# Performance work log

Measured on AMD Instinct MI355X. Metric: run time of the kernel, lower is better.

Reference implementation:

```python
import jax, jax.numpy as jnp
import numpy as np

B, S, E, H, BS = 4, 4096, 1024, 1024, 128  # batch, seq, embed, head_size, block_size


def setup_inputs() -> dict:
    key = jax.random.key(0)
    k1, k2, k3, k4 = jax.random.split(key, 4)
    x = jax.random.normal(k1, (B, S, E), dtype=jnp.float32)
    W_qkv = jax.random.normal(k2, (E, 3 * H), dtype=jnp.float32) * (E ** -0.5)
    W_out = jax.random.normal(k3, (H, H), dtype=jnp.float32) * (H ** -0.5)
    b_out = jax.random.normal(k4, (H,), dtype=jnp.float32) * 0.01
    return {"x": x, "W_qkv": W_qkv, "W_out": W_out, "b_out": b_out}


def reference(x, W_qkv, W_out, b_out):
    b, s, e = x.shape
    h = W_out.shape[1]
    nb = s // BS  # number of blocks (block-diagonal attention)
    qkv = x @ W_qkv                      # [B, S, 3H]
    q, k, v = jnp.split(qkv, 3, axis=-1)

    def blk(t):
        return t.reshape(b, nb, BS, h)   # [B, nb, BS, H]

    scale = h ** -0.5
    # each query block attends only its own key/value block
    scores = jnp.einsum('bnqd,bnkd->bnqk', blk(q), blk(k)) * scale  # [B, nb, BS, BS]
    causal = jnp.tril(jnp.ones((BS, BS), dtype=bool))  # diagonal block of full tril
    scores = jnp.where(causal, scores, -jnp.inf)
    scores = scores - jnp.max(scores, axis=-1, keepdims=True)
    p = jnp.exp(scores)
    p = p / (jnp.sum(p, axis=-1, keepdims=True) + 1e-6)  # faithful: softmax with +1e-6 eps
    out = jnp.einsum('bnqk,bnkd->bnqd', p, blk(v)).reshape(b, s, h)
    return out @ W_out.T + b_out
```

## Files before the change

### kernel.cpp

```cpp
#include <hip/hip_runtime.h>
#include <hip/hip_bf16.h>

typedef __attribute__((ext_vector_type(8))) short short8;
typedef __attribute__((ext_vector_type(4))) float float4_;

typedef const __attribute__((address_space(1))) void* gas_t;
typedef __attribute__((address_space(3))) void* las_t;

__device__ __forceinline__ void gl_lds16(const void* g, void* l) {
  __builtin_amdgcn_global_load_lds((gas_t)g, (las_t)l, 16, 0, 0);
}

__device__ __forceinline__ short f2b(float f) {
  union { __hip_bfloat16 h; short s; } u;
  u.h = __float2bfloat16(f);
  return u.s;
}
__device__ __forceinline__ short8 cvt8(float4_ lo, float4_ hi) {
  short8 r;
#pragma unroll
  for (int t = 0; t < 4; t++) { r[t] = f2b(lo[t]); r[t + 4] = f2b(hi[t]); }
  return r;
}

__global__ __launch_bounds__(256) void prep(
    const float* __restrict__ Wqkv, short* __restrict__ WqkvT,
    const float* __restrict__ Wout, short* __restrict__ Woutb,
    const float* __restrict__ x, short* __restrict__ xb, int has_x)
{
  __shared__ __align__(16) short T[64 * 72];
  const int b   = blockIdx.x;
  const int tid = threadIdx.x;
  if (b < 768) {
    const int R = 1024, C = 3072;
    const int r0 = (b / 48) * 64;
    const int c0 = (b % 48) * 64;
    const int r  = tid >> 2;
    const int cp = (tid & 3) * 16;
#pragma unroll
    for (int g = 0; g < 4; g++) {
      float4_ v = *(const float4_*)&Wqkv[(long)(r0 + r) * C + c0 + cp + g * 4];
#pragma unroll
      for (int t = 0; t < 4; t++) T[(cp + g * 4 + t) * 72 + r] = f2b(v[t]);
    }
    __syncthreads();
    const int c  = tid >> 2;
    const int rp = (tid & 3) * 16;
    short8 w0 = *(const short8*)&T[c * 72 + rp];
    short8 w1 = *(const short8*)&T[c * 72 + rp + 8];
    *(short8*)&WqkvT[(long)(c0 + c) * R + r0 + rp] = w0;
    *(short8*)&WqkvT[(long)(c0 + c) * R + r0 + rp + 8] = w1;
  } else if (b < 1280) {
    const long i = ((long)(b - 768) * 256 + tid) * 8;
    float4_ lo = *(const float4_*)&Wout[i];
    float4_ hi = *(const float4_*)&Wout[i + 4];
    *(short8*)&Woutb[i] = cvt8(lo, hi);
  } else if (has_x) {
    const long i = ((long)(b - 1280) * 256 + tid) * 8;
    float4_ lo = *(const float4_*)&x[i];
    float4_ hi = *(const float4_*)&x[i + 4];
    *(short8*)&xb[i] = cvt8(lo, hi);
  }
}

__global__ __launch_bounds__(256) void gemm_bt(
    const void* __restrict__ Av, int lda, int a_f32,
    const short* __restrict__ B,
    void* __restrict__ Cv, int ldc, int c_f32,
    int K, const float* __restrict__ bias)
{
  __shared__ __align__(16) short As[128 * 64];
  __shared__ __align__(16) short Bs[128 * 64];
  const int tid  = threadIdx.x;
  const int lane = tid & 63;
  const int w    = tid >> 6;
  const int quad = lane >> 4;
  const int l15  = lane & 15;
  const int wm   = (w >> 1) * 64;
  const int wn   = (w & 1) * 64;

  const int nx  = gridDim.x;
  const int nwg = nx * gridDim.y;
  int wid = blockIdx.y * nx + blockIdx.x;
  if ((nwg & 7) == 0) wid = (wid & 7) * (nwg >> 3) + (wid >> 3);
  const int m0 = (wid / nx) * 128;
  const int n0 = (wid % nx) * 128;

  float4_ acc[4][4] = {};

  const int srow = tid >> 3;
  const int sk   = tid & 7;
  const int kswz = ((sk ^ (srow & 7)) * 8);
  const int wbase = w * 512;
  const int frow = tid >> 1;
  const int fh   = tid & 1;
  const int swzc = quad ^ (l15 & 7);

  for (int k0 = 0; k0 < K; k0 += 64) {
    short8 fs[4];
    if (a_f32) {
      const float* Af = (const float*)Av;
#pragma unroll
      for (int g = 0; g < 2; g++) {
        float4_ v0 = *(const float4_*)&Af[(long)(m0 + frow) * lda + k0 + fh * 32 + g * 16];
        float4_ v1 = *(const float4_*)&Af[(long)(m0 + frow) * lda + k0 + fh * 32 + g * 16 + 4];
        float4_ v2 = *(const float4_*)&Af[(long)(m0 + frow) * lda + k0 + fh * 32 + g * 16 + 8];
        float4_ v3 = *(const float4_*)&Af[(long)(m0 + frow) * lda + k0 + fh * 32 + g * 16 + 12];
        fs[g * 2]     = cvt8(v0, v1);
        fs[g * 2 + 1] = cvt8(v2, v3);
      }
    }
    __syncthreads();
    if (a_f32) {
#pragma unroll
      for (int g = 0; g < 4; g++) {
        const int c_log = fh * 4 + g;
        *(short8*)&As[frow * 64 + ((c_log ^ (frow & 7)) * 8)] = fs[g];
      }
    } else {
      const short* Ab = (const short*)Av;
#pragma unroll
      for (int g = 0; g < 4; g++)
        gl_lds16(&Ab[(long)(m0 + g * 32 + srow) * lda + k0 + kswz],
                 &As[g * 2048 + wbase]);
    }
#pragma unroll
    for (int g = 0; g < 4; g++)
      gl_lds16(&B[(long)(n0 + g * 32 + srow) * K + k0 + kswz],
               &Bs[g * 2048 + wbase]);
    __syncthreads();
#pragma unroll
    for (int kk = 0; kk < 2; kk++) {
      short8 a[4], b[4];
      const int ch = (kk * 4) ^ swzc;
#pragma unroll
      for (int i = 0; i < 4; i++)
        a[i] = *(const short8*)&As[(wm + i * 16 + l15) * 64 + ((kk * 4 + quad) ^ (l15 & 7)) * 8];
#pragma unroll
      for (int j = 0; j < 4; j++)
        b[j] = *(const short8*)&Bs[(wn + j * 16 + l15) * 64 + ((kk * 4 + quad) ^ (l15 & 7)) * 8];
      (void)ch;
#pragma unroll
      for (int i = 0; i < 4; i++)
#pragma unroll
        for (int j = 0; j < 4; j++)
          acc[i][j] = __builtin_amdgcn_mfma_f32_16x16x32_bf16(a[i], b[j], acc[i][j], 0, 0, 0);
    }
  }

  const int gidx = w >> 1;
  for (int i = 0; i < 4; i++) {
    __syncthreads();
    if (c_f32) {
      float* scr = (float*)As;
#pragma unroll
      for (int j = 0; j < 4; j++) {
        const int col = wn + j * 16 + l15;
        const float bv = bias ? bias[n0 + col] : 0.0f;
#pragma unroll
        for (int r = 0; r < 4; r++) {
          const int row = gidx * 16 + quad * 4 + r;
          scr[row * 128 + (col ^ ((row & 7) << 4))] = acc[i][j][r] + bv;
        }
      }
    } else {
#pragma unroll
      for (int j = 0; j < 4; j++) {
        const int col = wn + j * 16 + l15;
#pragma unroll
        for (int r = 0; r < 4; r++) {
          const int row = gidx * 16 + quad * 4 + r;
          As[row * 128 + (col ^ ((row & 7) << 4))] = f2b(acc[i][j][r]);
        }
      }
    }
    __syncthreads();
    const int rs   = tid >> 3;
    const int colp = (tid & 7) * 16;
    const int cs   = colp ^ ((rs & 7) << 4);
    const long row_g = m0 + (rs >> 4) * 64 + i * 16 + (rs & 15);
    if (c_f32) {
      float* C = (float*)Cv;
      const float* scr = (const float*)As;
#pragma unroll
      for (int q = 0; q < 4; q++) {
        float4_ v = *(const float4_*)&scr[rs * 128 + cs + q * 4];
        *(float4_*)&C[row_g * ldc + n0 + colp + q * 4] = v;
      }
    } else {
      short* C = (short*)Cv;
      short8 v0 = *(const short8*)&As[rs * 128 + cs];
      short8 v1 = *(const short8*)&As[rs * 128 + cs + 8];
      *(short8*)&C[row_g * ldc + n0 + colp]     = v0;
      *(short8*)&C[row_g * ldc + n0 + colp + 8] = v1;
    }
  }
}

template<int NJ>
__device__ __forceinline__ void attn_body(short* __restrict__ qkv, int tile,
                                          short* smem)
{
  constexpr int NK    = NJ * 16;
  constexpr int STR   = NK + 8;
  constexpr int QROW0 = (NJ == 8) ? 64 : 0;
  short* Qs = smem;
  short* Ks = smem + 2048;
  short* Ps = Ks + NK * 32;
  short* Vt = Ps + 64 * STR;
  short* Ot = Vt + 64 * STR;

  const int tid  = threadIdx.x;
  const int lane = tid & 63;
  const int w    = tid >> 6;
  const int quad = lane >> 4;
  const int l15  = lane & 15;
  const long base = (long)tile * 128 * 3072;
  const int wbase = w * 512;

  const short* Qg = qkv + base + (long)QROW0 * 3072;
  const short* Kg = qkv + base + 1024;
  const short* Vg = qkv + base + 2048;

  float4_ acc[NJ] = {};
  const int srow = tid >> 2;
  const int kp   = (tid & 3) * 8;

  for (int k0 = 0; k0 < 1024; k0 += 32) {
    __syncthreads();
    gl_lds16(&Qg[(long)srow * 3072 + k0 + kp], &Qs[wbase]);
    gl_lds16(&Kg[(long)srow * 3072 + k0 + kp], &Ks[wbase]);
    if (NJ == 8)
      gl_lds16(&Kg[(long)(srow + 64) * 3072 + k0 + kp], &Ks[2048 + wbase]);
    __syncthreads();
    short8 a = *(const short8*)&Qs[(w * 16 + l15) * 32 + quad * 8];
#pragma unroll
    for (int j = 0; j < NJ; j++) {
      short8 b = *(const short8*)&Ks[(j * 16 + l15) * 32 + quad * 8];
      acc[j] = __builtin_amdgcn_mfma_f32_16x16x32_bf16(a, b, acc[j], 0, 0, 0);
    }
  }

  const float scale = 0.03125f;
#pragma unroll
  for (int r = 0; r < 4; r++) {
    const int rowq = w * 16 + quad * 4 + r;
    float s[NJ];
    float mx = -3.0e38f;
#pragma unroll
    for (int j = 0; j < NJ; j++) {
      const int col = j * 16 + l15;
      const float v = acc[j][r] * scale;
      s[j] = (col <= QROW0 + rowq) ? v : -3.0e38f;
      mx = fmaxf(mx, s[j]);
    }
    mx = fmaxf(mx, __shfl_xor(mx, 1));
    mx = fmaxf(mx, __shfl_xor(mx, 2));
    mx = fmaxf(mx, __shfl_xor(mx, 4));
    mx = fmaxf(mx, __shfl_xor(mx, 8));
    float p[NJ];
    float sum = 0.0f;
#pragma unroll
    for (int j = 0; j < NJ; j++) {
      p[j] = (s[j] > -1.0e38f) ? __expf(s[j] - mx) : 0.0f;
      sum += p[j];
    }
    sum += __shfl_xor(sum, 1);
    sum += __shfl_xor(sum, 2);
    sum += __shfl_xor(sum, 4);
    sum += __shfl_xor(sum, 8);
    const float inv = 1.0f / (sum + 1e-6f);
#pragma unroll
    for (int j = 0; j < NJ; j++)
      Ps[rowq * STR + j * 16 + l15] = f2b(p[j] * inv);
  }

  short* Op = qkv + base + (long)QROW0 * 3072;
  for (int d0 = 0; d0 < 1024; d0 += 64) {
    __syncthreads();
    if (NJ == 8) {
      const int kr = tid >> 1, dp = (tid & 1) * 32;
#pragma unroll
      for (int gg = 0; gg < 4; gg++) {
        short8 v = *(const short8*)&Vg[(long)kr * 3072 + d0 + dp + gg * 8];
#pragma unroll
        for (int t = 0; t < 8; t++) Vt[(dp + gg * 8 + t) * STR + kr] = v[t];
      }
    } else {
      const int kr = tid >> 2, dp = (tid & 3) * 16;
#pragma unroll
      for (int gg = 0; gg < 2; gg++) {
        short8 v = *(const short8*)&Vg[(long)kr * 3072 + d0 + dp + gg * 8];
#pragma unroll
        for (int t = 0; t < 8; t++) Vt[(dp + gg * 8 + t) * STR + kr] = v[t];
      }
    }
    __syncthreads();
    float4_ o[4] = {};
#pragma unroll
    for (int kk = 0; kk < NK / 32; kk++) {
      short8 a = *(const short8*)&Ps[(w * 16 + l15) * STR + kk * 32 + quad * 8];
#pragma unroll
      for (int j = 0; j < 4; j++) {
        short8 b = *(const short8*)&Vt[(j * 16 + l15) * STR + kk * 32 + quad * 8];
        o[j] = __builtin_amdgcn_mfma_f32_16x16x32_bf16(a, b, o[j], 0, 0, 0);
      }
    }
#pragma unroll
    for (int j = 0; j < 4; j++)
#pragma unroll
      for (int r = 0; r < 4; r++)
        Ot[(w * 16 + quad * 4 + r) * 72 + j * 16 + l15] = f2b(o[j][r]);
    __syncthreads();
    const int orow = tid >> 2, ocp = (tid & 3) * 16;
    short8 v0 = *(const short8*)&Ot[orow * 72 + ocp];
    short8 v1 = *(const short8*)&Ot[orow * 72 + ocp + 8];
    *(short8*)&Op[(long)orow * 3072 + d0 + ocp]     = v0;
    *(short8*)&Op[(long)orow * 3072 + d0 + ocp + 8] = v1;
  }
}

__global__ __launch_bounds__(256) void attn_blockdiag(short* __restrict__ qkv)
{
  __shared__ __align__(16) short smem[28160];
  const int tile = blockIdx.x >> 1;
  if (blockIdx.x & 1) attn_body<8>(qkv, tile, smem);
  else                attn_body<4>(qkv, tile, smem);
}

extern "C" void kernel_launch(void* const* d_in, const int* in_sizes, int n_in,
                              void* d_out, int out_size, void* d_ws, size_t ws_size,
                              hipStream_t stream) {
  const float* x    = (const float*)d_in[0];
  const float* Wqkv = (const float*)d_in[1];
  const float* Wout = (const float*)d_in[2];
  const float* bout = (const float*)d_in[3];
  float* out = (float*)d_out;

  char* ws = (char*)d_ws;
  short* WqkvT = (short*)ws;
  short* Woutb = (short*)(ws + 6291456);
  short* qkv   = (short*)(ws + 8388608);
  short* xb    = (short*)(ws + 8388608 + (size_t)16384 * 3072 * 2);

  if (ws_size >= 8388608 + (size_t)16384 * 3072 * 2 + (size_t)16384 * 1024 * 2) {
    prep<<<9472, 256, 0, stream>>>(Wqkv, WqkvT, Wout, Woutb, x, xb, 1);
    gemm_bt<<<dim3(24, 128), 256, 0, stream>>>(xb, 1024, 0, WqkvT,
                                               qkv, 3072, 0, 1024, nullptr);
    attn_blockdiag<<<dim3(256), 256, 0, stream>>>(qkv);
    gemm_bt<<<dim3(8, 128), 256, 0, stream>>>(qkv, 3072, 0, Woutb,
                                              out, 1024, 1, 1024, bout);
  } else if (ws_size >= 8388608 + (size_t)16384 * 3072 * 2) {
    prep<<<1280, 256, 0, stream>>>(Wqkv, WqkvT, Wout, Woutb, nullptr, nullptr, 0);
    gemm_bt<<<dim3(24, 128), 256, 0, stream>>>(x, 1024, 1, WqkvT,
                                               qkv, 3072, 0, 1024, nullptr);
    attn_blockdiag<<<dim3(256), 256, 0, stream>>>(qkv);
    gemm_bt<<<dim3(8, 128), 256, 0, stream>>>(qkv, 3072, 0, Woutb,
                                              out, 1024, 1, 1024, bout);
  } else {
    prep<<<1280, 256, 0, stream>>>(Wqkv, WqkvT, Wout, Woutb, nullptr, nullptr, 0);
    for (int c = 0; c < 4; c++) {
      const float* xc = x + (long)c * 4096 * 1024;
      float* outc = out + (long)c * 4096 * 1024;
      gemm_bt<<<dim3(24, 32), 256, 0, stream>>>(xc, 1024, 1, WqkvT,
                                                qkv, 3072, 0, 1024, nullptr);
      attn_blockdiag<<<dim3(64), 256, 0, stream>>>(qkv);
      gemm_bt<<<dim3(8, 32), 256, 0, stream>>>(qkv, 3072, 0, Woutb,
                                               outc, 1024, 1, 1024, bout);
    }
  }
}
```

Baseline: 345.9 us.

## Split attention head dimension across two warp groups with 512-thread blocks

The attention kernel now runs 512 threads per block, split into two 256-thread groups. Each group handles alternating 64-wide chunks of the head dimension for both the QK^T reduction and the PV output. Group partial scores are combined through shared memory before group 0 does the softmax. The Q/K staging also moves to 64-wide k-steps with XOR-swizzled LDS layouts, which halves the loop trip count. The aim is more parallelism in a kernel with only 256 blocks. The cost is more LDS use, an extra score-reduction pass, and half the threads idling during softmax.

```diff
diff --git a/kernel.cpp b/kernel.cpp
--- a/kernel.cpp
+++ b/kernel.cpp
@@ -94,7 +94,6 @@
   const int wbase = w * 512;
   const int frow = tid >> 1;
   const int fh   = tid & 1;
-  const int swzc = quad ^ (l15 & 7);
 
   for (int k0 = 0; k0 < K; k0 += 64) {
     short8 fs[4];
@@ -132,14 +131,12 @@
 #pragma unroll
     for (int kk = 0; kk < 2; kk++) {
       short8 a[4], b[4];
-      const int ch = (kk * 4) ^ swzc;
 #pragma unroll
       for (int i = 0; i < 4; i++)
         a[i] = *(const short8*)&As[(wm + i * 16 + l15) * 64 + ((kk * 4 + quad) ^ (l15 & 7)) * 8];
 #pragma unroll
       for (int j = 0; j < 4; j++)
         b[j] = *(const short8*)&Bs[(wn + j * 16 + l15) * 64 + ((kk * 4 + quad) ^ (l15 & 7)) * 8];
-      (void)ch;
 #pragma unroll
       for (int i = 0; i < 4; i++)
 #pragma unroll
@@ -202,107 +199,137 @@
                                           short* smem)
 {
   constexpr int NK    = NJ * 16;
-  constexpr int STR   = NK + 8;
   constexpr int QROW0 = (NJ == 8) ? 64 : 0;
-  short* Qs = smem;
-  short* Ks = smem + 2048;
-  short* Ps = Ks + NK * 32;
-  short* Vt = Ps + 64 * STR;
-  short* Ot = Vt + 64 * STR;
+  constexpr int KCALLS = NK / 32;
+
+  short* Ps = smem;
+  short* U  = smem + 8704;
 
   const int tid  = threadIdx.x;
+  const int t8   = tid & 255;
+  const int g    = tid >> 8;
+  const int wl   = (tid >> 6) & 3;
   const int lane = tid & 63;
-  const int w    = tid >> 6;
   const int quad = lane >> 4;
   const int l15  = lane & 15;
   const long base = (long)tile * 128 * 3072;
-  const int wbase = w * 512;
 
   const short* Qg = qkv + base + (long)QROW0 * 3072;
   const short* Kg = qkv + base + 1024;
   const short* Vg = qkv + base + 2048;
 
+  short* Qs = U + g * 4096;
+  short* Ks = U + 8192 + g * 8192;
+  const int srow8 = t8 >> 3;
+  const int sk    = t8 & 7;
+  const int kswz  = (sk ^ (srow8 & 7)) * 8;
+  const int wb    = wl * 512;
+
   float4_ acc[NJ] = {};
-  const int srow = tid >> 2;
-  const int kp   = (tid & 3) * 8;
-
-  for (int k0 = 0; k0 < 1024; k0 += 32) {
-    __syncthreads();
-    gl_lds16(&Qg[(long)srow * 3072 + k0 + kp], &Qs[wbase]);
-    gl_lds16(&Kg[(long)srow * 3072 + k0 + kp], &Ks[wbase]);
-    if (NJ == 8)
-      gl_lds16(&Kg[(long)(srow + 64) * 3072 + k0 + kp], &Ks[2048 + wbase]);
-    __syncthreads();
-    short8 a = *(const short8*)&Qs[(w * 16 + l15) * 32 + quad * 8];
-#pragma unroll
-    for (int j = 0; j < NJ; j++) {
-      short8 b = *(const short8*)&Ks[(j * 16 + l15) * 32 + quad * 8];
-      acc[j] = __builtin_amdgcn_mfma_f32_16x16x32_bf16(a, b, acc[j], 0, 0, 0);
-    }
-  }
-
-  const float scale = 0.03125f;
-#pragma unroll
-  for (int r = 0; r < 4; r++) {
-    const int rowq = w * 16 + quad * 4 + r;
-    float s[NJ];
-    float mx = -3.0e38f;
-#pragma unroll
-    for (int j = 0; j < NJ; j++) {
-      const int col = j * 16 + l15;
-      const float v = acc[j][r] * scale;
-      s[j] = (col <= QROW0 + rowq) ? v : -3.0e38f;
-      mx = fmaxf(mx, s[j]);
-    }
-    mx = fmaxf(mx, __shfl_xor(mx, 1));
-    mx = fmaxf(mx, __shfl_xor(mx, 2));
-    mx = fmaxf(mx, __shfl_xor(mx, 4));
-    mx = fmaxf(mx, __shfl_xor(mx, 8));
-    float p[NJ];
-    float sum = 0.0f;
-#pragma unroll
-    for (int j = 0; j < NJ; j++) {
-      p[j] = (s[j] > -1.0e38f) ? __expf(s[j] - mx) : 0.0f;
-      sum += p[j];
-    }
-    sum += __shfl_xor(sum, 1);
-    sum += __shfl_xor(sum, 2);
-    sum += __shfl_xor(sum, 4);
-    sum += __shfl_xor(sum, 8);
-    const float inv = 1.0f / (sum + 1e-6f);
-#pragma unroll
-    for (int j = 0; j < NJ; j++)
-      Ps[rowq * STR + j * 16 + l15] = f2b(p[j] * inv);
-  }
-
+
+  for (int i = 0; i < 8; i++) {
+    const int k0 = g * 64 + i * 128;
+    __syncthreads();
+#pragma unroll
+    for (int c = 0; c < 2; c++)
+      gl_lds16(&Qg[(long)(c * 32 + srow8) * 3072 + k0 + kswz], &Qs[c * 2048 + wb]);
+#pragma unroll
+    for (int c = 0; c < KCALLS; c++)
+      gl_lds16(&Kg[(long)(c * 32 + srow8) * 3072 + k0 + kswz], &Ks[c * 2048 + wb]);
+    __syncthreads();
+#pragma unroll
+    for (int kk = 0; kk < 2; kk++) {
+      const int ch = ((kk * 4 + quad) ^ (l15 & 7)) * 8;
+      short8 a = *(const short8*)&Qs[(wl * 16 + l15) * 64 + ch];
+#pragma unroll
+      for (int j = 0; j < NJ; j++) {
+        short8 b = *(const short8*)&Ks[(j * 16 + l15) * 64 + ch];
+        acc[j] = __builtin_amdgcn_mfma_f32_16x16x32_bf16(a, b, acc[j], 0, 0, 0);
+      }
+    }
+  }
+  __syncthreads();
+
+  float* Sscr = (float*)U;
+  if (g == 1) {
+#pragma unroll
+    for (int r = 0; r < 4; r++) {
+      const int rowq = wl * 16 + quad * 4 + r;
+#pragma unroll
+      for (int j = 0; j < NJ; j++)
+        Sscr[rowq * 132 + j * 16 + l15] = acc[j][r];
+    }
+  }
+  __syncthreads();
+  if (g == 0) {
+    const float scale = 0.03125f;
+#pragma unroll
+    for (int r = 0; r < 4; r++) {
+      const int rowq = wl * 16 + quad * 4 + r;
+      float s[NJ];
+      float mx = -3.0e38f;
+#pragma unroll
+      for (int j = 0; j < NJ; j++) {
+        const int col = j * 16 + l15;
+        const float v = (acc[j][r] + Sscr[rowq * 132 + col]) * scale;
+        s[j] = (col <= QROW0 + rowq) ? v : -3.0e38f;
+        mx = fmaxf(mx, s[j]);
+      }
+      mx = fmaxf(mx, __shfl_xor(mx, 1));
+      mx = fmaxf(mx, __shfl_xor(mx, 2));
+      mx = fmaxf(mx, __shfl_xor(mx, 4));
+      mx = fmaxf(mx, __shfl_xor(mx, 8));
+      float p[NJ];
+      float sum = 0.0f;
+#pragma unroll
+      for (int j = 0; j < NJ; j++) {
+        p[j] = (s[j] > -1.0e38f) ? __expf(s[j] - mx) : 0.0f;
+        sum += p[j];
+      }
+      sum += __shfl_xor(sum, 1);
+      sum += __shfl_xor(sum, 2);
+      sum += __shfl_xor(sum, 4);
+      sum += __shfl_xor(sum, 8);
+      const float inv = 1.0f / (sum + 1e-6f);
+#pragma unroll
+      for (int j = 0; j < NJ; j++)
+        Ps[rowq * 136 + j * 16 + l15] = f2b(p[j] * inv);
+    }
+  }
+  __syncthreads();
+
+  short* Vt = U + g * 8704;
+  short* Ot = U + 17408 + g * 4608;
   short* Op = qkv + base + (long)QROW0 * 3072;
-  for (int d0 = 0; d0 < 1024; d0 += 64) {
+
+  for (int i = 0; i < 8; i++) {
+    const int d0 = g * 64 + i * 128;
     __syncthreads();
     if (NJ == 8) {
-      const int kr = tid >> 1, dp = (tid & 1) * 32;
+      const int kr = t8 >> 1, dp = (t8 & 1) * 32;
 #pragma unroll
       for (int gg = 0; gg < 4; gg++) {
         short8 v = *(const short8*)&Vg[(long)kr * 3072 + d0 + dp + gg * 8];
 #pragma unroll
-        for (int t = 0; t < 8; t++) Vt[(dp + gg * 8 + t) * STR + kr] = v[t];
+        for (int t = 0; t < 8; t++) Vt[(dp + gg * 8 + t) * 136 + kr] = v[t];
       }
     } else {
-      const int kr = tid >> 2, dp = (tid & 3) * 16;
+      const int kr = t8 >> 2, dp = (t8 & 3) * 16;
 #pragma unroll
       for (int gg = 0; gg < 2; gg++) {
         short8 v = *(const short8*)&Vg[(long)kr * 3072 + d0 + dp + gg * 8];
 #pragma unroll
-        for (int t = 0; t < 8; t++) Vt[(dp + gg * 8 + t) * STR + kr] = v[t];
+        for (int t = 0; t < 8; t++) Vt[(dp + gg * 8 + t) * 136 + kr] = v[t];
       }
     }
     __syncthreads();
     float4_ o[4] = {};
 #pragma unroll
     for (int kk = 0; kk < NK / 32; kk++) {
-      short8 a = *(const short8*)&Ps[(w * 16 + l15) * STR + kk * 32 + quad * 8];
+      short8 a = *(const short8*)&Ps[(wl * 16 + l15) * 136 + kk * 32 + quad * 8];
 #pragma unroll
       for (int j = 0; j < 4; j++) {
-        short8 b = *(const short8*)&Vt[(j * 16 + l15) * STR + kk * 32 + quad * 8];
+        short8 b = *(const short8*)&Vt[(j * 16 + l15) * 136 + kk * 32 + quad * 8];
         o[j] = __builtin_amdgcn_mfma_f32_16x16x32_bf16(a, b, o[j], 0, 0, 0);
       }
     }
@@ -310,9 +337,9 @@
     for (int j = 0; j < 4; j++)
 #pragma unroll
       for (int r = 0; r < 4; r++)
-        Ot[(w * 16 + quad * 4 + r) * 72 + j * 16 + l15] = f2b(o[j][r]);
-    __syncthreads();
-    const int orow = tid >> 2, ocp = (tid & 3) * 16;
+        Ot[(wl * 16 + quad * 4 + r) * 72 + j * 16 + l15] = f2b(o[j][r]);
+    __syncthreads();
+    const int orow = t8 >> 2, ocp = (t8 & 3) * 16;
     short8 v0 = *(const short8*)&Ot[orow * 72 + ocp];
     short8 v1 = *(const short8*)&Ot[orow * 72 + ocp + 8];
     *(short8*)&Op[(long)orow * 3072 + d0 + ocp]     = v0;
@@ -320,9 +347,9 @@
   }
 }
 
-__global__ __launch_bounds__(256) void attn_blockdiag(short* __restrict__ qkv)
+__global__ __launch_bounds__(512) void attn_blockdiag(short* __restrict__ qkv)
 {
-  __shared__ __align__(16) short smem[28160];
+  __shared__ __align__(16) short smem[35328];
   const int tile = blockIdx.x >> 1;
   if (blockIdx.x & 1) attn_body<8>(qkv, tile, smem);
   else                attn_body<4>(qkv, tile, smem);
@@ -347,14 +374,14 @@
     prep<<<9472, 256, 0, stream>>>(Wqkv, WqkvT, Wout, Woutb, x, xb, 1);
     gemm_bt<<<dim3(24, 128), 256, 0, stream>>>(xb, 1024, 0, WqkvT,
                                                qkv, 3072, 0, 1024, nullptr);
-    attn_blockdiag<<<dim3(256), 256, 0, stream>>>(qkv);
+    attn_blockdiag<<<dim3(256), 512, 0, stream>>>(qkv);
     gemm_bt<<<dim3(8, 128), 256, 0, stream>>>(qkv, 3072, 0, Woutb,
                                               out, 1024, 1, 1024, bout);
   } else if (ws_size >= 8388608 + (size_t)16384 * 3072 * 2) {
     prep<<<1280, 256, 0, stream>>>(Wqkv, WqkvT, Wout, Woutb, nullptr, nullptr, 0);
     gemm_bt<<<dim3(24, 128), 256, 0, stream>>>(x, 1024, 1, WqkvT,
                                                qkv, 3072, 0, 1024, nullptr);
-    attn_blockdiag<<<dim3(256), 256, 0, stream>>>(qkv);
+    attn_blockdiag<<<dim3(256), 512, 0, stream>>>(qkv);
     gemm_bt<<<dim3(8, 128), 256, 0, stream>>>(qkv, 3072, 0, Woutb,
                                               out, 1024, 1, 1024, bout);
   } else {
@@ -364,7 +391,7 @@
       float* outc = out + (long)c * 4096 * 1024;
       gemm_bt<<<dim3(24, 32), 256, 0, stream>>>(xc, 1024, 1, WqkvT,
                                                 qkv, 3072, 0, 1024, nullptr);
-      attn_blockdiag<<<dim3(64), 256, 0, stream>>>(qkv);
+      attn_blockdiag<<<dim3(64), 512, 0, stream>>>(qkv);
       gemm_bt<<<dim3(8, 32), 256, 0, stream>>>(qkv, 3072, 0, Woutb,
                                                outc, 1024, 1, 1024, bout);
     }
```

Result: faster. 328.5 us (-5.0%).
